# Performance work log

Measured on AMD Instinct MI355X. Metric: run time of the kernel, lower is better.

The kernel has to match this reference:

```python
import jax, jax.numpy as jnp
import numpy as np

B, S, H, FF, E = 4, 4096, 1024, 4096, 8
EPS = 1e-5


def setup_inputs() -> dict:
    key = jax.random.key(0)
    ks = jax.random.split(key, 8)
    std = 0.02
    return {
        "x": jax.random.normal(ks[0], (B, S, H), jnp.float32),
        "norm_weight": jnp.ones((H,), jnp.float32),
        "router_w": jax.random.normal(ks[1], (E, H), jnp.float32) * std,
        "router_b": jnp.zeros((E,), jnp.float32),
        "fc1_w": jax.random.normal(ks[2], (E, FF, H), jnp.float32) * std,
        "fc1_b": jnp.zeros((E, FF), jnp.float32),
        "fc2_w": jax.random.normal(ks[3], (E, H, FF), jnp.float32) * std,
        "fc2_b": jnp.zeros((E, H), jnp.float32),
    }


def reference(x, norm_weight, router_w, router_b, fc1_w, fc1_b, fc2_w, fc2_b):
    b, s, h = x.shape
    T = b * s
    e = router_w.shape[0]
    cap = T // e  # expert capacity, capacity_factor = 1.0

    x_flat = x.reshape(T, h)
    # RMSNorm (pre-norm on MoE input)
    xn = x_flat * jax.lax.rsqrt(jnp.mean(x_flat * x_flat, axis=-1, keepdims=True) + EPS) * norm_weight

    # Router (no jitter: eval / jitter_noise=0)
    logits = xn @ router_w.T + router_b          # [T, E]
    probs = jax.nn.softmax(logits, axis=-1)       # [T, E]

    # Expert-choice routing: each expert picks its top-`cap` tokens by prob
    gates, idx = jax.lax.top_k(probs.T, cap)      # [E, cap], [E, cap]

    # Dispatch (gather) and grouped expert MLP
    xe = xn[idx]                                   # [E, cap, H]
    hmid = jnp.einsum('ech,efh->ecf', xe, fc1_w) + fc1_b[:, None, :]
    hmid = jax.nn.gelu(hmid, approximate=False)    # torch F.gelu default (exact)
    ye = jnp.einsum('ecf,ehf->ech', hmid, fc2_w) + fc2_b[:, None, :]

    # Combine: gated scatter-add back to token positions, normalize by gate sum
    flat_idx = idx.reshape(-1)                     # [E*cap]
    weighted = (ye * gates[..., None]).reshape(-1, h)
    out = jnp.zeros((T, h), x.dtype).at[flat_idx].add(weighted)
    gate_sums = jnp.zeros((T, 1), x.dtype).at[flat_idx].add(gates.reshape(-1, 1))
    out = out / jnp.maximum(gate_sums, 1e-9)       # unrouted tokens stay zero
    return out.reshape(b, s, h)
```

## Files before the change

kernel.cpp:

```cpp
#include <hip/hip_runtime.h>
#include <hip/hip_bf16.h>

#define T_TOK 16384
#define H_DIM 1024
#define FF_DIM 4096
#define NE 8
#define CAP 2048
#define EPS_F 1e-5f

#define BM2 256
#define BN2 256
#define BK2 32

typedef __attribute__((ext_vector_type(4))) float f32x4;
typedef __attribute__((ext_vector_type(8))) short bf16x8;
typedef unsigned long long u64;
typedef unsigned int u32;

__device__ inline void gload_lds16(const void* g, void* l) {
  __builtin_amdgcn_global_load_lds(
      (const __attribute__((address_space(1))) unsigned int*)g,
      (__attribute__((address_space(3))) unsigned int*)l, 16, 0, 0);
}

__device__ inline unsigned short bf16_bits(float f) {
  __hip_bfloat16 h = __float2bfloat16(f);
  unsigned short u;
  __builtin_memcpy(&u, &h, 2);
  return u;
}

__device__ inline float bits_f32(unsigned short u) {
  const u32 x = ((u32)u) << 16;
  float f;
  __builtin_memcpy(&f, &x, 4);
  return f;
}

__global__ __launch_bounds__(256) void router_kernel(
    const float* __restrict__ x, const float* __restrict__ nw,
    const float* __restrict__ rw, const float* __restrict__ rb,
    __hip_bfloat16* __restrict__ xn, u64* __restrict__ keys,
    int* __restrict__ tok_cnt,
    const float* __restrict__ w1s, __hip_bfloat16* __restrict__ w1d,
    const float* __restrict__ w2s, __hip_bfloat16* __restrict__ w2d, int do_cvt) {
  const int t = blockIdx.x;
  const int tid = threadIdx.x;
  if (tid == 0) tok_cnt[t] = 0;
  const float4 v = reinterpret_cast<const float4*>(x + (size_t)t * H_DIM)[tid];
  float ss = v.x * v.x + v.y * v.y + v.z * v.z + v.w * v.w;
#pragma unroll
  for (int o = 32; o > 0; o >>= 1) ss += __shfl_down(ss, o);
  __shared__ float red[4];
  __shared__ float redl[4][NE];
  const int wv = tid >> 6, ln = tid & 63;
  if (ln == 0) red[wv] = ss;
  __syncthreads();
  const float tot = red[0] + red[1] + red[2] + red[3];
  const float scale = rsqrtf(tot * (1.0f / H_DIM) + EPS_F);
  const float4 w4 = reinterpret_cast<const float4*>(nw)[tid];
  float xv0 = v.x * scale * w4.x, xv1 = v.y * scale * w4.y;
  float xv2 = v.z * scale * w4.z, xv3 = v.w * scale * w4.w;
  ushort4 u4;
  u4.x = bf16_bits(xv0); u4.y = bf16_bits(xv1);
  u4.z = bf16_bits(xv2); u4.w = bf16_bits(xv3);
  reinterpret_cast<ushort4*>(xn + (size_t)t * H_DIM)[tid] = u4;
  float lg[NE];
#pragma unroll
  for (int e = 0; e < NE; ++e) {
    const float4 r4 = reinterpret_cast<const float4*>(rw + (size_t)e * H_DIM)[tid];
    lg[e] = xv0 * r4.x + xv1 * r4.y + xv2 * r4.z + xv3 * r4.w;
  }
#pragma unroll
  for (int o = 32; o > 0; o >>= 1) {
#pragma unroll
    for (int e = 0; e < NE; ++e) lg[e] += __shfl_down(lg[e], o);
  }
  if (ln == 0) {
#pragma unroll
    for (int e = 0; e < NE; ++e) redl[wv][e] = lg[e];
  }
  __syncthreads();
  if (tid == 0) {
    float l[NE];
    float m = -1e30f;
#pragma unroll
    for (int e = 0; e < NE; ++e) {
      l[e] = redl[0][e] + redl[1][e] + redl[2][e] + redl[3][e] + rb[e];
      m = fmaxf(m, l[e]);
    }
    float s = 0.f;
#pragma unroll
    for (int e = 0; e < NE; ++e) { l[e] = expf(l[e] - m); s += l[e]; }
    const float inv = 1.0f / s;
#pragma unroll
    for (int e = 0; e < NE; ++e) {
      const float p = l[e] * inv;
      const u64 key = ((u64)__float_as_uint(p) << 32) | (u32)(0xFFFFFFFFu - (u32)t);
      keys[(size_t)e * T_TOK + t] = key;
    }
  }
  if (do_cvt) {
    const int n4each = NE * FF_DIM * H_DIM / 4;
    const int gstride = gridDim.x * blockDim.x;
    for (int i = blockIdx.x * blockDim.x + tid; i < 2 * n4each; i += gstride) {
      const float* s = (i < n4each) ? w1s : w2s;
      __hip_bfloat16* d = (i < n4each) ? w1d : w2d;
      const int j = (i < n4each) ? i : i - n4each;
      const float4 vv = reinterpret_cast<const float4*>(s)[j];
      ushort4 o;
      o.x = bf16_bits(vv.x); o.y = bf16_bits(vv.y);
      o.z = bf16_bits(vv.z); o.w = bf16_bits(vv.w);
      reinterpret_cast<ushort4*>(d)[j] = o;
    }
  }
}

#define EQCAP 7168
__global__ __launch_bounds__(1024) void topk_kernel(
    const u64* __restrict__ keys, int* __restrict__ idxl,
    float* __restrict__ gatel, int* __restrict__ tok_list, int* __restrict__ tok_cnt) {
  const int e = blockIdx.x;
  const int tid = threadIdx.x;
  const int lane = tid & 63;
  const u64* ke = keys + (size_t)e * T_TOK;
  __shared__ int hist[256];
  __shared__ u32 s_pref;
  __shared__ int s_k;
  __shared__ int s_cnt;
  __shared__ int s_eq;
  __shared__ u32 eqlist[EQCAP];

  u32 pref = 0;
  int pbits = 0;
  int kneed = CAP;
  for (int pass = 0; pass < 4; ++pass) {
    if (tid < 256) hist[tid] = 0;
    __syncthreads();
    const int shift = 24 - 8 * pass;
    for (int i = tid; i < T_TOK; i += 1024) {
      const u32 hi = (u32)(ke[i] >> 32);
      const bool ok = (pbits == 0) || ((hi >> (32 - pbits)) == pref);
      const int d = ok ? (int)((hi >> shift) & 255) : -1;
      u64 act = __ballot(ok);
      while (act) {
        const int src = __ffsll((long long)act) - 1;
        const int dl = __shfl(d, src);
        const u64 mb = __ballot(ok && (d == dl));
        if (lane == src) atomicAdd(&hist[dl], (int)__popcll(mb));
        act &= ~mb;
      }
    }
    __syncthreads();
    if (tid == 0) {
      int cum = 0;
      int d = 255;
      for (; d >= 0; --d) {
        cum += hist[d];
        if (cum >= kneed) break;
      }
      s_k = kneed - (cum - hist[d]);
      s_pref = (pref << 8) | (u32)d;
    }
    __syncthreads();
    pref = s_pref;
    kneed = s_k;
    pbits += 8;
    __syncthreads();
  }
  const u32 thrp = pref;
  const float thrp_f = __uint_as_float(thrp);

  if (tid == 0) { s_cnt = 0; s_eq = 0; }
  __syncthreads();
  for (int i = tid; i < T_TOK; i += 1024) {
    const u64 key = ke[i];
    const u32 hi = (u32)(key >> 32);
    if (hi > thrp) {
      const int pos = atomicAdd(&s_cnt, 1);
      if (pos < CAP) {
        const int tok = (int)(0xFFFFFFFFu - (u32)key);
        idxl[e * CAP + pos] = tok;
        gatel[e * CAP + pos] = __uint_as_float(hi);
        const int j = atomicAdd(tok_cnt + tok, 1);
        if (j < NE) tok_list[tok * NE + j] = e * CAP + pos;
      }
    } else if (hi == thrp) {
      const int j = atomicAdd(&s_eq, 1);
      if (j < EQCAP) eqlist[j] = (u32)key;
    }
  }
  __syncthreads();
  const int neq = s_eq;
  if (neq <= EQCAP) {
    u32 prefl = 0;
    int pb = 0;
    int kn = kneed;
    if (neq > kneed) {
      for (int pass = 0; pass < 4; ++pass) {
        if (tid < 256) hist[tid] = 0;
        __syncthreads();
        const int shift = 24 - 8 * pass;
        for (int i = tid; i < neq; i += 1024) {
          const u32 vv = eqlist[i];
          if ((pb == 0) || ((vv >> (32 - pb)) == prefl)) atomicAdd(&hist[(vv >> shift) & 255], 1);
        }
        __syncthreads();
        if (tid == 0) {
          int cum = 0;
          int d = 255;
          for (; d >= 0; --d) {
            cum += hist[d];
            if (cum >= kn) break;
          }
          s_k = kn - (cum - hist[d]);
          s_pref = (prefl << 8) | (u32)d;
        }
        __syncthreads();
        prefl = s_pref;
        kn = s_k;
        pb += 8;
        __syncthreads();
      }
    }
    for (int i = tid; i < neq; i += 1024) {
      const u32 lo = eqlist[i];
      if (neq <= kneed || lo >= prefl) {
        const int pos = atomicAdd(&s_cnt, 1);
        if (pos < CAP) {
          const int tok = (int)(0xFFFFFFFFu - lo);
          idxl[e * CAP + pos] = tok;
          gatel[e * CAP + pos] = thrp_f;
          const int j = atomicAdd(tok_cnt + tok, 1);
          if (j < NE) tok_list[tok * NE + j] = e * CAP + pos;
        }
      }
    }
  } else {
    u64 pref64 = (u64)thrp;
    int pb64 = 32;
    int kn = kneed;
    for (int pass = 4; pass < 8; ++pass) {
      if (tid < 256) hist[tid] = 0;
      __syncthreads();
      const int shift = 56 - 8 * pass;
      for (int i = tid; i < T_TOK; i += 1024) {
        const u64 key = ke[i];
        if ((key >> (64 - pb64)) == pref64) atomicAdd(&hist[(int)((key >> shift) & 255)], 1);
      }
      __syncthreads();
      if (tid == 0) {
        int cum = 0;
        int d = 255;
        for (; d >= 0; --d) {
          cum += hist[d];
          if (cum >= kn) break;
        }
        s_k = kn - (cum - hist[d]);
        s_pref = (u32)d;
      }
      __syncthreads();
      pref64 = (pref64 << 8) | s_pref;
      kn = s_k;
      pb64 += 8;
      __syncthreads();
    }
    for (int i = tid; i < T_TOK; i += 1024) {
      const u64 key = ke[i];
      if ((u32)(key >> 32) == thrp && key >= pref64) {
        const int pos = atomicAdd(&s_cnt, 1);
        if (pos < CAP) {
          const int tok = (int)(0xFFFFFFFFu - (u32)key);
          idxl[e * CAP + pos] = tok;
          gatel[e * CAP + pos] = thrp_f;
          const int j = atomicAdd(tok_cnt + tok, 1);
          if (j < NE) tok_list[tok * NE + j] = e * CAP + pos;
        }
      }
    }
  }
}

__global__ __launch_bounds__(256) void cvt2_kernel(
    const float* __restrict__ s1, __hip_bfloat16* __restrict__ d1,
    const float* __restrict__ s2, __hip_bfloat16* __restrict__ d2, int n4each) {
  int i = blockIdx.x * blockDim.x + threadIdx.x;
  const int stride = gridDim.x * blockDim.x;
  for (; i < 2 * n4each; i += stride) {
    const float* s = (i < n4each) ? s1 : s2;
    __hip_bfloat16* d = (i < n4each) ? d1 : d2;
    const int j = (i < n4each) ? i : i - n4each;
    const float4 v = reinterpret_cast<const float4*>(s)[j];
    ushort4 o;
    o.x = bf16_bits(v.x); o.y = bf16_bits(v.y);
    o.z = bf16_bits(v.z); o.w = bf16_bits(v.w);
    reinterpret_cast<ushort4*>(d)[j] = o;
  }
}

template <int MODE>
__global__ __launch_bounds__(1024) void gemm7_kernel(
    const __hip_bfloat16* __restrict__ Asrc, const __hip_bfloat16* __restrict__ Bw,
    const float* __restrict__ bias, const int* __restrict__ idxl,
    const float* __restrict__ gatel, __hip_bfloat16* __restrict__ hmid,
    __hip_bfloat16* __restrict__ ye, int ebase) {
  constexpr int N = (MODE == 0) ? FF_DIM : H_DIM;
  constexpr int K = (MODE == 0) ? H_DIM : FF_DIM;
  constexpr int NBN = N / BN2;
  constexpr int LOG_NBN = (MODE == 0) ? 4 : 2;
  constexpr int BPE = (CAP / BM2) * NBN;
  constexpr int LOG_BPE = (MODE == 0) ? 7 : 5;
  constexpr int NT = K / BK2;

  const int nwg = gridDim.x;
  const int wg0 = blockIdx.x;
  const int wg = (wg0 & 7) * (nwg >> 3) + (wg0 >> 3);
  const int z = wg >> LOG_BPE;
  const int rr = wg & (BPE - 1);
  const int bm = rr >> LOG_NBN;
  const int bn = rr & (NBN - 1);
  const int e = ebase + z;

  const int tid = threadIdx.x;
  const int lane = tid & 63;
  const int w = tid >> 6;
  const int wr = w >> 2, wc = w & 3;
  const int fr = lane & 15, q = lane >> 4;

  __shared__ char smem[131072];

  const int srow = tid >> 2;
  const int sg = tid & 3;
  const int skoff = (sg ^ ((srow >> 1) & 3)) * 8;

  const __hip_bfloat16* asrc;
  if constexpr (MODE == 0) {
    const int t0 = idxl[e * CAP + bm * BM2 + srow];
    asrc = Asrc + (size_t)t0 * H_DIM + skoff;
  } else {
    asrc = Asrc + ((size_t)z * CAP + bm * BM2 + srow) * FF_DIM + skoff;
  }
  const __hip_bfloat16* bsrc = Bw + (size_t)z * N * K + (size_t)(bn * BN2 + srow) * K + skoff;

  const int slotk = ((q ^ ((fr >> 1) & 3)) << 4);
  const int aoff0 = (wr * 64 + fr) * 64 + slotk;
  const int boff0 = 16384 + (wc * 64 + fr) * 64 + slotk;

  f32x4 acc[4][4] = {};
  bf16x8 Af[4], Bf[4];

#define GLDA(sb, k0) gload_lds16(asrc + (k0), smem + (sb)*32768 + tid * 16)
#define GLDB(sb, k0) gload_lds16(bsrc + (k0), smem + (sb)*32768 + 16384 + tid * 16)

  GLDA(0, 0); GLDB(0, 0);
  GLDA(1, BK2); GLDB(1, BK2);
  GLDA(2, 2 * BK2); GLDB(2, 2 * BK2);
  asm volatile("s_waitcnt vmcnt(4)");
  __builtin_amdgcn_s_barrier();
  __builtin_amdgcn_sched_barrier(0);

  for (int kt = 0; kt < NT; ++kt) {
    const int cur = kt & 3;
    const int kref = (kt + 3 < NT) ? (kt + 3) : (kt + 3 - NT);
    const int k0p = kref * BK2;
    const int psl = (kt + 3) & 3;
    const char* base = smem + cur * 32768;

    Af[0] = *reinterpret_cast<const bf16x8*>(base + aoff0);
    Af[1] = *reinterpret_cast<const bf16x8*>(base + aoff0 + 1024);
    Af[2] = *reinterpret_cast<const bf16x8*>(base + aoff0 + 2048);
    Af[3] = *reinterpret_cast<const bf16x8*>(base + aoff0 + 3072);
    Bf[0] = *reinterpret_cast<const bf16x8*>(base + boff0);
    Bf[1] = *reinterpret_cast<const bf16x8*>(base + boff0 + 1024);
    __builtin_amdgcn_sched_barrier(0);
    Bf[2] = *reinterpret_cast<const bf16x8*>(base + boff0 + 2048);
    Bf[3] = *reinterpret_cast<const bf16x8*>(base + boff0 + 3072);
    GLDA(psl, k0p);
    asm volatile("s_waitcnt vmcnt(3)");
    __builtin_amdgcn_s_barrier();
    asm volatile("s_waitcnt lgkmcnt(2)");
    __builtin_amdgcn_sched_barrier(0);
    __builtin_amdgcn_s_setprio(1);
#pragma unroll
    for (int m_ = 0; m_ < 4; ++m_) {
      acc[m_][0] = __builtin_amdgcn_mfma_f32_16x16x32_bf16(Af[m_], Bf[0], acc[m_][0], 0, 0, 0);
      acc[m_][1] = __builtin_amdgcn_mfma_f32_16x16x32_bf16(Af[m_], Bf[1], acc[m_][1], 0, 0, 0);
    }
    __builtin_amdgcn_s_setprio(0);
    __builtin_amdgcn_sched_barrier(0);

    GLDB(psl, k0p);
    asm volatile("s_waitcnt lgkmcnt(0)");
    __builtin_amdgcn_sched_barrier(0);
    __builtin_amdgcn_s_barrier();
    __builtin_amdgcn_sched_barrier(0);
    __builtin_amdgcn_s_setprio(1);
#pragma unroll
    for (int m_ = 0; m_ < 4; ++m_) {
      acc[m_][2] = __builtin_amdgcn_mfma_f32_16x16x32_bf16(Af[m_], Bf[2], acc[m_][2], 0, 0, 0);
      acc[m_][3] = __builtin_amdgcn_mfma_f32_16x16x32_bf16(Af[m_], Bf[3], acc[m_][3], 0, 0, 0);
    }
    __builtin_amdgcn_s_setprio(0);
    __builtin_amdgcn_sched_barrier(0);
  }
#undef GLDA
#undef GLDB

  if constexpr (MODE == 0) {
#pragma unroll
    for (int m = 0; m < 4; ++m) {
      const int rbase = bm * BM2 + wr * 64 + m * 16 + q * 4;
#pragma unroll
      for (int n = 0; n < 4; ++n) {
        const int gn = bn * BN2 + wc * 64 + n * 16 + fr;
        const float bb = bias[e * FF_DIM + gn];
#pragma unroll
        for (int i = 0; i < 4; ++i) {
          const float v = acc[m][n][i] + bb;
          const float u = v * (1.5957691216f + 0.0713548162972f * v * v);
          const float s = 1.0f / (1.0f + __expf(-u));
          hmid[((size_t)z * CAP + rbase + i) * FF_DIM + gn] = __float2bfloat16(v * s);
        }
      }
    }
  } else {
#pragma unroll
    for (int m = 0; m < 4; ++m) {
      const int rbase = bm * BM2 + wr * 64 + m * 16 + q * 4;
      float gt[4];
#pragma unroll
      for (int i = 0; i < 4; ++i) gt[i] = gatel[e * CAP + rbase + i];
#pragma unroll
      for (int n = 0; n < 4; ++n) {
        const int gn = bn * BN2 + wc * 64 + n * 16 + fr;
        const float bb = bias[e * H_DIM + gn];
#pragma unroll
        for (int i = 0; i < 4; ++i)
          ye[((size_t)e * CAP + rbase + i) * H_DIM + gn] =
              __float2bfloat16((acc[m][n][i] + bb) * gt[i]);
      }
    }
  }
}

__global__ __launch_bounds__(256) void combine_kernel(
    const __hip_bfloat16* __restrict__ ye, const float* __restrict__ gatel,
    const int* __restrict__ tok_list, const int* __restrict__ tok_cnt,
    float* __restrict__ out) {
  const int t = blockIdx.x;
  const int tid = threadIdx.x;
  const int cnt = tok_cnt[t];
  float a0 = 0.f, a1 = 0.f, a2 = 0.f, a3 = 0.f, gs = 0.f;
  for (int j = 0; j < cnt && j < NE; ++j) {
    const int ent = tok_list[t * NE + j];
    gs += gatel[ent];
    const ushort4 v = reinterpret_cast<const ushort4*>(ye + (size_t)ent * H_DIM)[tid];
    a0 += bits_f32(v.x);
    a1 += bits_f32(v.y);
    a2 += bits_f32(v.z);
    a3 += bits_f32(v.w);
  }
  const float inv = 1.0f / fmaxf(gs, 1e-9f);
  float4 o;
  o.x = a0 * inv; o.y = a1 * inv; o.z = a2 * inv; o.w = a3 * inv;
  reinterpret_cast<float4*>(out + (size_t)t * H_DIM)[tid] = o;
}

extern "C" void kernel_launch(void* const* d_in, const int* in_sizes, int n_in,
                              void* d_out, int out_size, void* d_ws, size_t ws_size,
                              hipStream_t stream) {
  const float* x = (const float*)d_in[0];
  const float* nw = (const float*)d_in[1];
  const float* rw = (const float*)d_in[2];
  const float* rb = (const float*)d_in[3];
  const float* fc1w = (const float*)d_in[4];
  const float* fc1b = (const float*)d_in[5];
  const float* fc2w = (const float*)d_in[6];
  const float* fc2b = (const float*)d_in[7];
  float* out = (float*)d_out;

  char* ws = (char*)d_ws;
  size_t off = 0;
  auto alloc = [&](size_t b) {
    char* p = ws + off;
    off += (b + 255) & ~(size_t)255;
    return p;
  };
  __hip_bfloat16* xn = (__hip_bfloat16*)alloc((size_t)T_TOK * H_DIM * 2);
  u64* keys = (u64*)alloc((size_t)NE * T_TOK * 8);
  int* idxl = (int*)alloc((size_t)NE * CAP * 4);
  float* gatel = (float*)alloc((size_t)NE * CAP * 4);
  int* tok_list = (int*)alloc((size_t)T_TOK * NE * 4);
  int* tok_cnt = (int*)alloc((size_t)T_TOK * 4);
  __hip_bfloat16* ye = (__hip_bfloat16*)alloc((size_t)NE * CAP * H_DIM * 2);

  int EC = NE;
  while (EC > 1) {
    const size_t per = (size_t)EC * ((size_t)FF_DIM * H_DIM * 2 * 2 + (size_t)CAP * FF_DIM * 2);
    if (off + per + 4096 <= ws_size) break;
    EC >>= 1;
  }
  __hip_bfloat16* w1b = (__hip_bfloat16*)alloc((size_t)EC * FF_DIM * H_DIM * 2);
  __hip_bfloat16* w2b = (__hip_bfloat16*)alloc((size_t)EC * H_DIM * FF_DIM * 2);
  __hip_bfloat16* hmid = (__hip_bfloat16*)alloc((size_t)EC * CAP * FF_DIM * 2);

  const int fused_cvt = (EC == NE) ? 1 : 0;

  router_kernel<<<T_TOK, 256, 0, stream>>>(x, nw, rw, rb, xn, keys, tok_cnt,
                                           fc1w, w1b, fc2w, w2b, fused_cvt);
  topk_kernel<<<NE, 1024, 0, stream>>>(keys, idxl, gatel, tok_list, tok_cnt);

  for (int eb = 0; eb < NE; eb += EC) {
    if (!fused_cvt) {
      const int n4 = EC * FF_DIM * H_DIM / 4;
      cvt2_kernel<<<4096, 256, 0, stream>>>(fc1w + (size_t)eb * FF_DIM * H_DIM, w1b,
                                            fc2w + (size_t)eb * H_DIM * FF_DIM, w2b, n4);
    }
    const int nb1 = EC * (CAP / BM2) * (FF_DIM / BN2);
    gemm7_kernel<0><<<nb1, 1024, 0, stream>>>(xn, w1b, fc1b, idxl, gatel, hmid, ye, eb);
    const int nb2 = EC * (CAP / BM2) * (H_DIM / BN2);
    gemm7_kernel<1><<<nb2, 1024, 0, stream>>>(hmid, w2b, fc2b, idxl, gatel, hmid, ye, eb);
  }
  combine_kernel<<<T_TOK, 256, 0, stream>>>(ye, gatel, tok_list, tok_cnt, out);
}
```

Baseline: 505.3 us.

## Rewrite expert GEMMs with 512-thread blocks, BK=64 and larger per-wave tiles

Replaces the 1024-thread, BK=32, 4-stage GEMM with a 512-thread kernel that uses BK=64 and double-buffered 64KB LDS stages. Each wave now computes a 128x64 output tile in four quadrant phases, with A and B sub-tile loads interleaved between the MFMA groups. The aim is more MFMA work per LDS read and fewer loop-iteration barriers. The cost is higher register pressure, fewer waves per CU to hide latency, and more barriers within each iteration.

```diff
diff --git a/kernel.cpp b/kernel.cpp
--- a/kernel.cpp
+++ b/kernel.cpp
@@ -10,7 +10,7 @@
 
 #define BM2 256
 #define BN2 256
-#define BK2 32
+#define BK3 64
 
 typedef __attribute__((ext_vector_type(4))) float f32x4;
 typedef __attribute__((ext_vector_type(8))) short bf16x8;
@@ -299,7 +299,7 @@
 }
 
 template <int MODE>
-__global__ __launch_bounds__(1024) void gemm7_kernel(
+__global__ __launch_bounds__(512, 2) void gemm15_kernel(
     const __hip_bfloat16* __restrict__ Asrc, const __hip_bfloat16* __restrict__ Bw,
     const float* __restrict__ bias, const int* __restrict__ idxl,
     const float* __restrict__ gatel, __hip_bfloat16* __restrict__ hmid,
@@ -310,7 +310,7 @@
   constexpr int LOG_NBN = (MODE == 0) ? 4 : 2;
   constexpr int BPE = (CAP / BM2) * NBN;
   constexpr int LOG_BPE = (MODE == 0) ? 7 : 5;
-  constexpr int NT = K / BK2;
+  constexpr int NT = K / BK3;
 
   const int nwg = gridDim.x;
   const int wg0 = blockIdx.x;
@@ -329,94 +329,172 @@
 
   __shared__ char smem[131072];
 
-  const int srow = tid >> 2;
-  const int sg = tid & 3;
-  const int skoff = (sg ^ ((srow >> 1) & 3)) * 8;
-
-  const __hip_bfloat16* asrc;
+  const int sr = tid >> 3;
+  const int sg = tid & 7;
+  const int skz = (sg ^ (sr & 7)) * 8;
+
+  const __hip_bfloat16 *as0, *as1, *as2, *as3;
   if constexpr (MODE == 0) {
-    const int t0 = idxl[e * CAP + bm * BM2 + srow];
-    asrc = Asrc + (size_t)t0 * H_DIM + skoff;
+    as0 = Asrc + (size_t)idxl[e * CAP + bm * BM2 + sr] * H_DIM + skz;
+    as1 = Asrc + (size_t)idxl[e * CAP + bm * BM2 + 64 + sr] * H_DIM + skz;
+    as2 = Asrc + (size_t)idxl[e * CAP + bm * BM2 + 128 + sr] * H_DIM + skz;
+    as3 = Asrc + (size_t)idxl[e * CAP + bm * BM2 + 192 + sr] * H_DIM + skz;
   } else {
-    asrc = Asrc + ((size_t)z * CAP + bm * BM2 + srow) * FF_DIM + skoff;
-  }
-  const __hip_bfloat16* bsrc = Bw + (size_t)z * N * K + (size_t)(bn * BN2 + srow) * K + skoff;
-
-  const int slotk = ((q ^ ((fr >> 1) & 3)) << 4);
-  const int aoff0 = (wr * 64 + fr) * 64 + slotk;
-  const int boff0 = 16384 + (wc * 64 + fr) * 64 + slotk;
-
-  f32x4 acc[4][4] = {};
-  bf16x8 Af[4], Bf[4];
-
-#define GLDA(sb, k0) gload_lds16(asrc + (k0), smem + (sb)*32768 + tid * 16)
-#define GLDB(sb, k0) gload_lds16(bsrc + (k0), smem + (sb)*32768 + 16384 + tid * 16)
-
-  GLDA(0, 0); GLDB(0, 0);
-  GLDA(1, BK2); GLDB(1, BK2);
-  GLDA(2, 2 * BK2); GLDB(2, 2 * BK2);
+    as0 = Asrc + ((size_t)z * CAP + bm * BM2 + sr) * FF_DIM + skz;
+    as1 = as0 + (size_t)64 * FF_DIM;
+    as2 = as0 + (size_t)128 * FF_DIM;
+    as3 = as0 + (size_t)192 * FF_DIM;
+  }
+  const __hip_bfloat16* bs0 = Bw + (size_t)z * N * K + (size_t)(bn * BN2 + sr) * K + skz;
+  const __hip_bfloat16* bs1 = bs0 + (size_t)64 * K;
+  const __hip_bfloat16* bs2 = bs0 + (size_t)128 * K;
+  const __hip_bfloat16* bs3 = bs0 + (size_t)192 * K;
+
+#define ST_AT(b, kt)                                            \
+  do {                                                          \
+    char* d_ = smem + (b)*65536 + tid * 16;                     \
+    gload_lds16(as0 + (kt)*BK3, d_);                            \
+    gload_lds16(as1 + (kt)*BK3, d_ + 8192);                     \
+  } while (0)
+#define ST_AB(b, kt)                                            \
+  do {                                                          \
+    char* d_ = smem + (b)*65536 + 16384 + tid * 16;             \
+    gload_lds16(as2 + (kt)*BK3, d_);                            \
+    gload_lds16(as3 + (kt)*BK3, d_ + 8192);                     \
+  } while (0)
+#define ST_BT(b, kt)                                            \
+  do {                                                          \
+    char* d_ = smem + (b)*65536 + 32768 + tid * 16;             \
+    gload_lds16(bs0 + (kt)*BK3, d_);                            \
+    gload_lds16(bs1 + (kt)*BK3, d_ + 8192);                     \
+  } while (0)
+#define ST_BB(b, kt)                                            \
+  do {                                                          \
+    char* d_ = smem + (b)*65536 + 49152 + tid * 16;             \
+    gload_lds16(bs2 + (kt)*BK3, d_);                            \
+    gload_lds16(bs3 + (kt)*BK3, d_ + 8192);                     \
+  } while (0)
+
+  const int kx0 = ((q) ^ (fr & 7)) << 4;
+  const int kx1 = ((4 + q) ^ (fr & 7)) << 4;
+  const int abase = wr * 16384 + fr * 128;
+  const int bbase = 32768 + (wc >> 1) * 16384 + ((wc & 1) * 64 + fr) * 128;
+
+  f32x4 acc[8][4] = {};
+  bf16x8 Aa[4][2], Ab[4][2], Bc[2][2], Bd[2][2];
+
+  ST_AT(0, 0); ST_AB(0, 0); ST_BT(0, 0); ST_BB(0, 0);
+  ST_BT(1, (NT > 1) ? 1 : 0); ST_BB(1, (NT > 1) ? 1 : 0);
   asm volatile("s_waitcnt vmcnt(4)");
   __builtin_amdgcn_s_barrier();
   __builtin_amdgcn_sched_barrier(0);
 
   for (int kt = 0; kt < NT; ++kt) {
-    const int cur = kt & 3;
-    const int kref = (kt + 3 < NT) ? (kt + 3) : (kt + 3 - NT);
-    const int k0p = kref * BK2;
-    const int psl = (kt + 3) & 3;
-    const char* base = smem + cur * 32768;
-
-    Af[0] = *reinterpret_cast<const bf16x8*>(base + aoff0);
-    Af[1] = *reinterpret_cast<const bf16x8*>(base + aoff0 + 1024);
-    Af[2] = *reinterpret_cast<const bf16x8*>(base + aoff0 + 2048);
-    Af[3] = *reinterpret_cast<const bf16x8*>(base + aoff0 + 3072);
-    Bf[0] = *reinterpret_cast<const bf16x8*>(base + boff0);
-    Bf[1] = *reinterpret_cast<const bf16x8*>(base + boff0 + 1024);
-    __builtin_amdgcn_sched_barrier(0);
-    Bf[2] = *reinterpret_cast<const bf16x8*>(base + boff0 + 2048);
-    Bf[3] = *reinterpret_cast<const bf16x8*>(base + boff0 + 3072);
-    GLDA(psl, k0p);
-    asm volatile("s_waitcnt vmcnt(3)");
-    __builtin_amdgcn_s_barrier();
-    asm volatile("s_waitcnt lgkmcnt(2)");
+    const int cb = kt & 1, nb = cb ^ 1;
+    const int kA = (kt + 1 < NT) ? kt + 1 : 0;
+    const int kB = (kt + 2 < NT) ? kt + 2 : kt + 2 - NT;
+    const char* base = smem + cb * 65536;
+
+#pragma unroll
+    for (int i = 0; i < 4; ++i) {
+      Aa[i][0] = *reinterpret_cast<const bf16x8*>(base + abase + i * 2048 + kx0);
+      Aa[i][1] = *reinterpret_cast<const bf16x8*>(base + abase + i * 2048 + kx1);
+    }
+#pragma unroll
+    for (int j = 0; j < 2; ++j) {
+      Bc[j][0] = *reinterpret_cast<const bf16x8*>(base + bbase + j * 2048 + kx0);
+      Bc[j][1] = *reinterpret_cast<const bf16x8*>(base + bbase + j * 2048 + kx1);
+    }
+    ST_AT(nb, kA);
+    __builtin_amdgcn_s_barrier();
+    asm volatile("s_waitcnt lgkmcnt(0)");
     __builtin_amdgcn_sched_barrier(0);
     __builtin_amdgcn_s_setprio(1);
 #pragma unroll
-    for (int m_ = 0; m_ < 4; ++m_) {
-      acc[m_][0] = __builtin_amdgcn_mfma_f32_16x16x32_bf16(Af[m_], Bf[0], acc[m_][0], 0, 0, 0);
-      acc[m_][1] = __builtin_amdgcn_mfma_f32_16x16x32_bf16(Af[m_], Bf[1], acc[m_][1], 0, 0, 0);
-    }
+    for (int i = 0; i < 4; ++i)
+#pragma unroll
+      for (int j = 0; j < 2; ++j) {
+        acc[i][j] = __builtin_amdgcn_mfma_f32_16x16x32_bf16(Aa[i][0], Bc[j][0], acc[i][j], 0, 0, 0);
+        acc[i][j] = __builtin_amdgcn_mfma_f32_16x16x32_bf16(Aa[i][1], Bc[j][1], acc[i][j], 0, 0, 0);
+      }
     __builtin_amdgcn_s_setprio(0);
     __builtin_amdgcn_sched_barrier(0);
-
-    GLDB(psl, k0p);
+    __builtin_amdgcn_s_barrier();
+
+#pragma unroll
+    for (int i = 0; i < 4; ++i) {
+      Ab[i][0] = *reinterpret_cast<const bf16x8*>(base + abase + 8192 + i * 2048 + kx0);
+      Ab[i][1] = *reinterpret_cast<const bf16x8*>(base + abase + 8192 + i * 2048 + kx1);
+    }
+    ST_AB(nb, kA);
+    __builtin_amdgcn_s_barrier();
     asm volatile("s_waitcnt lgkmcnt(0)");
     __builtin_amdgcn_sched_barrier(0);
-    __builtin_amdgcn_s_barrier();
-    __builtin_amdgcn_sched_barrier(0);
     __builtin_amdgcn_s_setprio(1);
 #pragma unroll
-    for (int m_ = 0; m_ < 4; ++m_) {
-      acc[m_][2] = __builtin_amdgcn_mfma_f32_16x16x32_bf16(Af[m_], Bf[2], acc[m_][2], 0, 0, 0);
-      acc[m_][3] = __builtin_amdgcn_mfma_f32_16x16x32_bf16(Af[m_], Bf[3], acc[m_][3], 0, 0, 0);
-    }
+    for (int i = 0; i < 4; ++i)
+#pragma unroll
+      for (int j = 0; j < 2; ++j) {
+        acc[4 + i][j] = __builtin_amdgcn_mfma_f32_16x16x32_bf16(Ab[i][0], Bc[j][0], acc[4 + i][j], 0, 0, 0);
+        acc[4 + i][j] = __builtin_amdgcn_mfma_f32_16x16x32_bf16(Ab[i][1], Bc[j][1], acc[4 + i][j], 0, 0, 0);
+      }
     __builtin_amdgcn_s_setprio(0);
     __builtin_amdgcn_sched_barrier(0);
-  }
-#undef GLDA
-#undef GLDB
+    __builtin_amdgcn_s_barrier();
+
+#pragma unroll
+    for (int j = 0; j < 2; ++j) {
+      Bd[j][0] = *reinterpret_cast<const bf16x8*>(base + bbase + 4096 + j * 2048 + kx0);
+      Bd[j][1] = *reinterpret_cast<const bf16x8*>(base + bbase + 4096 + j * 2048 + kx1);
+    }
+    __builtin_amdgcn_s_barrier();
+    asm volatile("s_waitcnt lgkmcnt(0)");
+    __builtin_amdgcn_sched_barrier(0);
+    __builtin_amdgcn_s_setprio(1);
+#pragma unroll
+    for (int i = 0; i < 4; ++i)
+#pragma unroll
+      for (int j = 0; j < 2; ++j) {
+        acc[i][2 + j] = __builtin_amdgcn_mfma_f32_16x16x32_bf16(Aa[i][0], Bd[j][0], acc[i][2 + j], 0, 0, 0);
+        acc[i][2 + j] = __builtin_amdgcn_mfma_f32_16x16x32_bf16(Aa[i][1], Bd[j][1], acc[i][2 + j], 0, 0, 0);
+      }
+    __builtin_amdgcn_s_setprio(0);
+    __builtin_amdgcn_sched_barrier(0);
+    __builtin_amdgcn_s_barrier();
+
+    ST_BT(cb, kB);
+    ST_BB(cb, kB);
+    asm volatile("s_waitcnt vmcnt(4)");
+    __builtin_amdgcn_s_barrier();
+    __builtin_amdgcn_sched_barrier(0);
+    __builtin_amdgcn_s_setprio(1);
+#pragma unroll
+    for (int i = 0; i < 4; ++i)
+#pragma unroll
+      for (int j = 0; j < 2; ++j) {
+        acc[4 + i][2 + j] = __builtin_amdgcn_mfma_f32_16x16x32_bf16(Ab[i][0], Bd[j][0], acc[4 + i][2 + j], 0, 0, 0);
+        acc[4 + i][2 + j] = __builtin_amdgcn_mfma_f32_16x16x32_bf16(Ab[i][1], Bd[j][1], acc[4 + i][2 + j], 0, 0, 0);
+      }
+    __builtin_amdgcn_s_setprio(0);
+    __builtin_amdgcn_sched_barrier(0);
+    __builtin_amdgcn_s_barrier();
+  }
+#undef ST_AT
+#undef ST_AB
+#undef ST_BT
+#undef ST_BB
 
   if constexpr (MODE == 0) {
 #pragma unroll
-    for (int m = 0; m < 4; ++m) {
-      const int rbase = bm * BM2 + wr * 64 + m * 16 + q * 4;
-#pragma unroll
-      for (int n = 0; n < 4; ++n) {
-        const int gn = bn * BN2 + wc * 64 + n * 16 + fr;
+    for (int mi = 0; mi < 8; ++mi) {
+      const int rbase = bm * BM2 + wr * 128 + mi * 16 + q * 4;
+#pragma unroll
+      for (int nj = 0; nj < 4; ++nj) {
+        const int gn = bn * BN2 + wc * 64 + nj * 16 + fr;
         const float bb = bias[e * FF_DIM + gn];
 #pragma unroll
         for (int i = 0; i < 4; ++i) {
-          const float v = acc[m][n][i] + bb;
+          const float v = acc[mi][nj][i] + bb;
           const float u = v * (1.5957691216f + 0.0713548162972f * v * v);
           const float s = 1.0f / (1.0f + __expf(-u));
           hmid[((size_t)z * CAP + rbase + i) * FF_DIM + gn] = __float2bfloat16(v * s);
@@ -425,19 +503,19 @@
     }
   } else {
 #pragma unroll
-    for (int m = 0; m < 4; ++m) {
-      const int rbase = bm * BM2 + wr * 64 + m * 16 + q * 4;
+    for (int mi = 0; mi < 8; ++mi) {
+      const int rbase = bm * BM2 + wr * 128 + mi * 16 + q * 4;
       float gt[4];
 #pragma unroll
       for (int i = 0; i < 4; ++i) gt[i] = gatel[e * CAP + rbase + i];
 #pragma unroll
-      for (int n = 0; n < 4; ++n) {
-        const int gn = bn * BN2 + wc * 64 + n * 16 + fr;
+      for (int nj = 0; nj < 4; ++nj) {
+        const int gn = bn * BN2 + wc * 64 + nj * 16 + fr;
         const float bb = bias[e * H_DIM + gn];
 #pragma unroll
         for (int i = 0; i < 4; ++i)
           ye[((size_t)e * CAP + rbase + i) * H_DIM + gn] =
-              __float2bfloat16((acc[m][n][i] + bb) * gt[i]);
+              __float2bfloat16((acc[mi][nj][i] + bb) * gt[i]);
       }
     }
   }
@@ -517,9 +595,9 @@
                                             fc2w + (size_t)eb * H_DIM * FF_DIM, w2b, n4);
     }
     const int nb1 = EC * (CAP / BM2) * (FF_DIM / BN2);
-    gemm7_kernel<0><<<nb1, 1024, 0, stream>>>(xn, w1b, fc1b, idxl, gatel, hmid, ye, eb);
+    gemm15_kernel<0><<<nb1, 512, 0, stream>>>(xn, w1b, fc1b, idxl, gatel, hmid, ye, eb);
     const int nb2 = EC * (CAP / BM2) * (H_DIM / BN2);
-    gemm7_kernel<1><<<nb2, 1024, 0, stream>>>(hmid, w2b, fc2b, idxl, gatel, hmid, ye, eb);
+    gemm15_kernel<1><<<nb2, 512, 0, stream>>>(hmid, w2b, fc2b, idxl, gatel, hmid, ye, eb);
   }
   combine_kernel<<<T_TOK, 256, 0, stream>>>(ye, gatel, tok_list, tok_cnt, out);
 }
```

Result: no change. 508.7 us (+0.7%).
